# Kernel optimization log

Measured on AMD Instinct MI355X. Metric: run time of the kernel, lower is better.

The kernel has to match this reference:

```python
import jax, jax.numpy as jnp
import numpy as np

# -------- problem dimensions (match init_kwargs / input_specs) --------
B, N, D = 4, 16384, 64          # batch, nodes (=128*128 pixels), feature dim
Q = 128                         # plateau/propagation state width (hardcoded in forward)
W = H = 128                     # grid (hardcoded in forward)
E = 131072                      # edges per batch element
M = 4                           # num_masks = k_nodes - 1
NUM_ITERS = 25                  # GraphPropagator(num_iters=25)
ADJ_THRESH = 0.5                # GraphPropagator(adj_thresh=0.5)


def setup_inputs() -> dict:
    key = jax.random.key(0)
    k1, k2, k3, k4 = jax.random.split(key, 4)
    node_features = jax.random.normal(k1, (B, N, D), dtype=jnp.float32)
    # global node indices in [0, B*N) -- the torch code concatenates per-batch
    # edge lists directly into a (B*N, B*N) SparseTensor
    node_edges = jax.random.randint(k2, (B, 2, E), 0, B * N)
    node_weights = jax.random.uniform(k3, (B, E), dtype=jnp.float32)
    init_state = jax.random.normal(k4, (B, N, Q), dtype=jnp.float32)
    return {"node_features": node_features, "node_edges": node_edges,
            "node_weights": node_weights, "init_state": init_state}


def _propagate(init_state, rows, cols, ws):
    """25-iteration sparse label propagation on the global (B*N,B*N) graph."""
    h = init_state.reshape(B * N, Q)

    def step(h, _):
        msg = ws[:, None] * h[cols]                                  # gather  [B*E, Q]
        agg = jax.ops.segment_sum(msg, rows, num_segments=B * N)    # scatter [B*N, Q]
        hn = agg / (jnp.linalg.norm(agg, axis=-1, keepdims=True) + 1e-8)
        return hn, None

    h, _ = jax.lax.scan(step, h, None, length=NUM_ITERS)
    return h  # [B*N, Q]


def _competition(platmap):
    """Competition(num_masks=M): agents claim pixels by plateau-vector affinity;
    an extra zero-logit background channel yields the unharvested mask."""
    flat = platmap.reshape(B, W * H, Q)
    agent_idx = jnp.linspace(0, W * H - 1, M).astype(jnp.int32)      # deterministic agent pixels
    agents = flat[:, agent_idx, :]                                   # [B, M, Q]
    logits = jnp.einsum('bnq,bmq->bnm', flat, agents) / jnp.sqrt(jnp.float32(Q))
    logits_ext = jnp.concatenate([logits, jnp.zeros((B, W * H, 1), logits.dtype)], axis=-1)
    probs = jax.nn.softmax(logits_ext, axis=-1)                      # [B, WH, M+1]
    masks = probs[..., :M].reshape(B, W, H, M)
    unharv = probs[..., M:].reshape(B, W, H, 1)
    alive = jnp.ones((B, M, 1), dtype=platmap.dtype)
    pheno = agents
    return masks, agents, alive, pheno, unharv


def reference(node_features, node_edges, node_weights, init_state):
    rows = node_edges[:, 0, :].reshape(-1)                           # [B*E] global row idx
    cols = node_edges[:, 1, :].reshape(-1)
    ws = node_weights.reshape(-1)
    ws = jnp.where(ws > ADJ_THRESH, ws, jnp.float32(0.0))            # adjacency threshold

    prop = _propagate(init_state, rows, cols, ws)                    # [B*N, Q]
    platmap = prop.reshape(B, W, H, Q)

    masks, agents, alive, pheno, unharv = _competition(platmap)
    masks_ext = jnp.concatenate([masks, unharv], axis=-1)            # [B, W, H, M+1]
    masks_ext = jnp.transpose(masks_ext, (0, 3, 1, 2))               # [B, M+1, W, H]

    nf = jnp.einsum('bnd,bmn->bmd', node_features,
                    masks_ext.reshape(B, M + 1, W * H))              # [B, M+1, D]
    # F.normalize(p=2, dim=1, eps=1e-12)
    nf = nf / jnp.clip(jnp.linalg.norm(nf, axis=1, keepdims=True), 1e-12)
    node_scores = jnp.max(masks_ext, axis=(-1, -2))                  # [B, M+1]
    return nf, masks_ext, node_scores
```

## Files before the change

### kernel.cpp

```cpp
#include <hip/hip_runtime.h>

#define B_    4
#define N_    16384
#define D_    64
#define Q_    128
#define E_    131072
#define M_    4
#define BN    65536
#define TOTE  524288
#define ITERS 25
#define PAD_CAP (TOTE + 3 * BN + 64)

#define OFF_MASKS 1280
#define OFF_SCORES 328960

__constant__ int c_agidx[4] = {0, 5461, 10922, 16383};

__device__ __forceinline__ unsigned pack_bf16x2(float x, float y) {
    unsigned ux = __float_as_uint(x);
    unsigned uy = __float_as_uint(y);
    ux = (ux + 0x7fffu + ((ux >> 16) & 1u)) >> 16;
    uy = (uy + 0x7fffu + ((uy >> 16) & 1u)) & 0xffff0000u;
    return ux | uy;
}

__global__ void k_count(const int* __restrict__ edges, const float* __restrict__ wts,
                        int* __restrict__ deg) {
    int idx = blockIdx.x * blockDim.x + threadIdx.x;
    if (idx >= TOTE) return;
    int b = idx >> 17;
    int e = idx & (E_ - 1);
    float w = wts[idx];
    if (w > 0.5f) {
        int row = edges[(b * 2) * E_ + e];
        atomicAdd(&deg[row], 1);
    }
}

__global__ __launch_bounds__(256) void k_scan1(const int* __restrict__ deg,
                                               int* __restrict__ blockSums) {
    int i = blockIdx.x * 256 + threadIdx.x;
    int v = (deg[i] + 3) & ~3;
    #pragma unroll
    for (int off = 1; off < 64; off <<= 1) v += __shfl_xor(v, off, 64);
    __shared__ int ws[4];
    int lane = threadIdx.x & 63, w = threadIdx.x >> 6;
    if (lane == 0) ws[w] = v;
    __syncthreads();
    if (threadIdx.x == 0)
        blockSums[blockIdx.x] = ws[0] + ws[1] + ws[2] + ws[3];
}

__global__ __launch_bounds__(256) void k_scan3(const int* __restrict__ deg,
                                               const int* __restrict__ blockSums,
                                               int* __restrict__ row_start,
                                               int* __restrict__ cursor) {
    int t = threadIdx.x;
    int lane = t & 63, w = t >> 6;
    __shared__ int offs[256];
    __shared__ int wtotA[4];
    __shared__ int wtotB[4];

    int bs = blockSums[t];
    int binc = bs;
    #pragma unroll
    for (int off = 1; off < 64; off <<= 1) {
        int u = __shfl_up(binc, off, 64);
        if (lane >= off) binc += u;
    }
    if (lane == 63) wtotA[w] = binc;
    __syncthreads();
    int badd = 0;
    for (int j = 0; j < w; ++j) badd += wtotA[j];
    offs[t] = binc + badd - bs;
    if (blockIdx.x == 0 && t == 255) row_start[BN] = binc + badd;
    __syncthreads();
    int blockOff = offs[blockIdx.x];

    int i = blockIdx.x * 256 + t;
    int v = (deg[i] + 3) & ~3;
    int incl = v;
    #pragma unroll
    for (int off = 1; off < 64; off <<= 1) {
        int u = __shfl_up(incl, off, 64);
        if (lane >= off) incl += u;
    }
    if (lane == 63) wtotB[w] = incl;
    __syncthreads();
    int wadd = 0;
    for (int j = 0; j < w; ++j) wadd += wtotB[j];
    int rs = blockOff + wadd + incl - v;
    row_start[i] = rs;
    cursor[i] = rs;
}

__global__ void k_scatter(const int* __restrict__ edges, const float* __restrict__ wts,
                          int* __restrict__ cursor, int2* __restrict__ cw) {
    int idx = blockIdx.x * blockDim.x + threadIdx.x;
    if (idx >= TOTE) return;
    int b = idx >> 17;
    int e = idx & (E_ - 1);
    float w = wts[idx];
    if (w > 0.5f) {
        int row = edges[(b * 2) * E_ + e];
        int col = edges[(b * 2) * E_ + E_ + e];
        int pos = atomicAdd(&cursor[row], 1);
        cw[pos] = make_int2(col, __float_as_int(w));
    }
}

__global__ void k_sort(const int* __restrict__ row_start, const int* __restrict__ deg,
                       int2* __restrict__ cw) {
    int n = blockIdx.x * blockDim.x + threadIdx.x;
    if (n >= BN) return;
    int s = row_start[n], epos = s + deg[n], pend = row_start[n + 1];
    for (int i = s + 1; i < epos; ++i) {
        int2 v = cw[i];
        unsigned long long key =
            ((unsigned long long)(unsigned)v.x << 32) | (unsigned)v.y;
        int j = i - 1;
        while (j >= s) {
            int2 u = cw[j];
            unsigned long long kj =
                ((unsigned long long)(unsigned)u.x << 32) | (unsigned)u.y;
            if (kj <= key) break;
            cw[j + 1] = u;
            --j;
        }
        cw[j + 1] = v;
    }
    for (int i = epos; i < pend; ++i) cw[i] = make_int2(0, 0);
}

__global__ __launch_bounds__(256) void k_hist(const int* __restrict__ deg,
                                              int* __restrict__ hist) {
    __shared__ int lh[256];
    int t = threadIdx.x;
    lh[t] = 0;
    __syncthreads();
    int n = blockIdx.x * 256 + t;
    int c = (deg[n] + 3) >> 2;
    if (c > 255) c = 255;
    atomicAdd(&lh[c], 1);
    __syncthreads();
    int cnt = lh[t];
    if (cnt) atomicAdd(&hist[t], cnt);
}

__global__ __launch_bounds__(256) void k_bucketscan(const int* __restrict__ hist,
                                                    int* __restrict__ bucketCur) {
    int t = threadIdx.x;
    int lane = t & 63, w = t >> 6;
    int v = hist[t];
    int incl = v;
    #pragma unroll
    for (int off = 1; off < 64; off <<= 1) {
        int u = __shfl_up(incl, off, 64);
        if (lane >= off) incl += u;
    }
    __shared__ int wtot[4];
    if (lane == 63) wtot[w] = incl;
    __syncthreads();
    int wadd = 0;
    for (int j = 0; j < w; ++j) wadd += wtot[j];
    bucketCur[t] = incl + wadd - v;
}

__global__ __launch_bounds__(256) void k_permscatter(const int* __restrict__ deg,
                                                     int* __restrict__ bucketCur,
                                                     int* __restrict__ perm) {
    __shared__ int lh[256];
    __shared__ int lbase[256];
    int t = threadIdx.x;
    lh[t] = 0;
    __syncthreads();
    int n = blockIdx.x * 256 + t;
    int c = (deg[n] + 3) >> 2;
    if (c > 255) c = 255;
    int lpos = atomicAdd(&lh[c], 1);
    __syncthreads();
    int cnt = lh[t];
    lbase[t] = cnt ? atomicAdd(&bucketCur[t], cnt) : 0;
    __syncthreads();
    perm[lbase[c] + lpos] = n;
}

__global__ __launch_bounds__(256) void k_pscan1(const int* __restrict__ deg,
                                                const int* __restrict__ perm,
                                                int* __restrict__ blockSums2) {
    int i = blockIdx.x * 256 + threadIdx.x;
    int v = (deg[perm[i]] + 3) & ~3;
    #pragma unroll
    for (int off = 1; off < 64; off <<= 1) v += __shfl_xor(v, off, 64);
    __shared__ int ws[4];
    int lane = threadIdx.x & 63, w = threadIdx.x >> 6;
    if (lane == 0) ws[w] = v;
    __syncthreads();
    if (threadIdx.x == 0)
        blockSums2[blockIdx.x] = ws[0] + ws[1] + ws[2] + ws[3];
}

__global__ __launch_bounds__(256) void k_pscan3(const int* __restrict__ deg,
                                                const int* __restrict__ perm,
                                                const int* __restrict__ blockSums2,
                                                int* __restrict__ prow) {
    int t = threadIdx.x;
    int lane = t & 63, w = t >> 6;
    __shared__ int offs[256];
    __shared__ int wtotA[4];
    __shared__ int wtotB[4];

    int bs = blockSums2[t];
    int binc = bs;
    #pragma unroll
    for (int off = 1; off < 64; off <<= 1) {
        int u = __shfl_up(binc, off, 64);
        if (lane >= off) binc += u;
    }
    if (lane == 63) wtotA[w] = binc;
    __syncthreads();
    int badd = 0;
    for (int j = 0; j < w; ++j) badd += wtotA[j];
    offs[t] = binc + badd - bs;
    if (blockIdx.x == 0 && t == 255) prow[BN] = binc + badd;
    __syncthreads();
    int blockOff = offs[blockIdx.x];

    int i = blockIdx.x * 256 + t;
    int v = (deg[perm[i]] + 3) & ~3;
    int incl = v;
    #pragma unroll
    for (int off = 1; off < 64; off <<= 1) {
        int u = __shfl_up(incl, off, 64);
        if (lane >= off) incl += u;
    }
    if (lane == 63) wtotB[w] = incl;
    __syncthreads();
    int wadd = 0;
    for (int j = 0; j < w; ++j) wadd += wtotB[j];
    prow[i] = blockOff + wadd + incl - v;
}

__global__ __launch_bounds__(256) void k_copy(const int* __restrict__ row_start,
                                              const int* __restrict__ prow,
                                              const int* __restrict__ perm,
                                              const int* __restrict__ deg,
                                              const int2* __restrict__ cw,
                                              int2* __restrict__ cw2) {
    int i = blockIdx.x * 256 + threadIdx.x;
    int n = perm[i];
    int src = row_start[n];
    int dst = prow[i];
    int nq = (deg[n] + 3) >> 2;
    for (int j = 0; j < nq; ++j) {
        const int4* s = (const int4*)(cw + src + (j << 2));
        int4* d = (int4*)(cw2 + dst + (j << 2));
        int4 x0 = s[0], x1 = s[1];
        d[0] = x0; d[1] = x1;
    }
}

template <bool F32IN>
__global__ __launch_bounds__(256) void k_prop(const void* __restrict__ hin,
                                              unsigned* __restrict__ hout,
                                              const int* __restrict__ prow,
                                              const int2* __restrict__ cw,
                                              const int* __restrict__ perm) {
    int lane = threadIdx.x & 63;
    int gid = (blockIdx.x << 2) + (threadIdx.x >> 6);
    int base = __builtin_amdgcn_readfirstlane(gid << 2);
    const int4 p4 = *(const int4*)(perm + base);
    int u0 = __builtin_amdgcn_readfirstlane(p4.x);
    int u1 = __builtin_amdgcn_readfirstlane(p4.y);
    int u2 = __builtin_amdgcn_readfirstlane(p4.z);
    int u3 = __builtin_amdgcn_readfirstlane(p4.w);
    int s0 = prow[base], s1 = prow[base + 1], s2 = prow[base + 2],
        s3 = prow[base + 3], e3 = prow[base + 4];
    int c0 = (s1 - s0) >> 2, c1 = (s2 - s1) >> 2;
    int c2 = (s3 - s2) >> 2, c3 = (e3 - s3) >> 2;
    int m01 = c0 > c1 ? c0 : c1, m23 = c2 > c3 ? c2 : c3;
    int nmax = m01 > m23 ? m01 : m23;
    int b0 = c0 ? s0 : 0, b1 = c1 ? s1 : 0, b2 = c2 ? s2 : 0, b3 = c3 ? s3 : 0;
    int l0 = (c0 ? c0 : 1) - 1, l1 = (c1 ? c1 : 1) - 1;
    int l2 = (c2 ? c2 : 1) - 1, l3 = (c3 ? c3 : 1) - 1;

    auto gather = [&](int col) -> float2 {
        if constexpr (F32IN) {
            return ((const float2*)hin)[((size_t)col << 6) + lane];
        } else {
            unsigned p = ((const unsigned*)hin)[((size_t)col << 6) + lane];
            float2 r;
            r.x = __uint_as_float(p << 16);
            r.y = __uint_as_float(p & 0xffff0000u);
            return r;
        }
    };

    float ax0 = 0.f, ay0 = 0.f, ax1 = 0.f, ay1 = 0.f;
    float ax2 = 0.f, ay2 = 0.f, ax3 = 0.f, ay3 = 0.f;
    for (int j = 0; j < nmax; ++j) {
        int j0 = j < l0 ? j : l0, j1 = j < l1 ? j : l1;
        int j2 = j < l2 ? j : l2, j3 = j < l3 ? j : l3;
        const int4* q0 = (const int4*)(cw + b0 + (j0 << 2));
        const int4* q1 = (const int4*)(cw + b1 + (j1 << 2));
        const int4* q2 = (const int4*)(cw + b2 + (j2 << 2));
        const int4* q3 = (const int4*)(cw + b3 + (j3 << 2));
        int4 a0 = q0[0], a1 = q0[1];
        int4 a2 = q1[0], a3 = q1[1];
        int4 a4 = q2[0], a5 = q2[1];
        int4 a6 = q3[0], a7 = q3[1];
        float2 v00 = gather(a0.x), v01 = gather(a0.z);
        float2 v02 = gather(a1.x), v03 = gather(a1.z);
        float2 v10 = gather(a2.x), v11 = gather(a2.z);
        float2 v12 = gather(a3.x), v13 = gather(a3.z);
        float2 v20 = gather(a4.x), v21 = gather(a4.z);
        float2 v22 = gather(a5.x), v23 = gather(a5.z);
        float2 v30 = gather(a6.x), v31 = gather(a6.z);
        float2 v32 = gather(a7.x), v33 = gather(a7.z);
        bool k0 = j < c0, k1 = j < c1, k2 = j < c2, k3 = j < c3;
        float w00 = k0 ? __int_as_float(a0.y) : 0.f;
        float w01 = k0 ? __int_as_float(a0.w) : 0.f;
        float w02 = k0 ? __int_as_float(a1.y) : 0.f;
        float w03 = k0 ? __int_as_float(a1.w) : 0.f;
        float w10 = k1 ? __int_as_float(a2.y) : 0.f;
        float w11 = k1 ? __int_as_float(a2.w) : 0.f;
        float w12 = k1 ? __int_as_float(a3.y) : 0.f;
        float w13 = k1 ? __int_as_float(a3.w) : 0.f;
        float w20 = k2 ? __int_as_float(a4.y) : 0.f;
        float w21 = k2 ? __int_as_float(a4.w) : 0.f;
        float w22 = k2 ? __int_as_float(a5.y) : 0.f;
        float w23 = k2 ? __int_as_float(a5.w) : 0.f;
        float w30 = k3 ? __int_as_float(a6.y) : 0.f;
        float w31 = k3 ? __int_as_float(a6.w) : 0.f;
        float w32 = k3 ? __int_as_float(a7.y) : 0.f;
        float w33 = k3 ? __int_as_float(a7.w) : 0.f;
        ax0 = fmaf(w00, v00.x, ax0); ay0 = fmaf(w00, v00.y, ay0);
        ax0 = fmaf(w01, v01.x, ax0); ay0 = fmaf(w01, v01.y, ay0);
        ax0 = fmaf(w02, v02.x, ax0); ay0 = fmaf(w02, v02.y, ay0);
        ax0 = fmaf(w03, v03.x, ax0); ay0 = fmaf(w03, v03.y, ay0);
        ax1 = fmaf(w10, v10.x, ax1); ay1 = fmaf(w10, v10.y, ay1);
        ax1 = fmaf(w11, v11.x, ax1); ay1 = fmaf(w11, v11.y, ay1);
        ax1 = fmaf(w12, v12.x, ax1); ay1 = fmaf(w12, v12.y, ay1);
        ax1 = fmaf(w13, v13.x, ax1); ay1 = fmaf(w13, v13.y, ay1);
        ax2 = fmaf(w20, v20.x, ax2); ay2 = fmaf(w20, v20.y, ay2);
        ax2 = fmaf(w21, v21.x, ax2); ay2 = fmaf(w21, v21.y, ay2);
        ax2 = fmaf(w22, v22.x, ax2); ay2 = fmaf(w22, v22.y, ay2);
        ax2 = fmaf(w23, v23.x, ax2); ay2 = fmaf(w23, v23.y, ay2);
        ax3 = fmaf(w30, v30.x, ax3); ay3 = fmaf(w30, v30.y, ay3);
        ax3 = fmaf(w31, v31.x, ax3); ay3 = fmaf(w31, v31.y, ay3);
        ax3 = fmaf(w32, v32.x, ax3); ay3 = fmaf(w32, v32.y, ay3);
        ax3 = fmaf(w33, v33.x, ax3); ay3 = fmaf(w33, v33.y, ay3);
    }
    float ss0 = ax0 * ax0 + ay0 * ay0;
    float ss1 = ax1 * ax1 + ay1 * ay1;
    float ss2 = ax2 * ax2 + ay2 * ay2;
    float ss3 = ax3 * ax3 + ay3 * ay3;
    #pragma unroll
    for (int off = 32; off; off >>= 1) {
        ss0 += __shfl_xor(ss0, off, 64);
        ss1 += __shfl_xor(ss1, off, 64);
        ss2 += __shfl_xor(ss2, off, 64);
        ss3 += __shfl_xor(ss3, off, 64);
    }
    float i0 = 1.0f / (sqrtf(ss0) + 1e-8f);
    float i1 = 1.0f / (sqrtf(ss1) + 1e-8f);
    float i2 = 1.0f / (sqrtf(ss2) + 1e-8f);
    float i3 = 1.0f / (sqrtf(ss3) + 1e-8f);
    hout[((size_t)u0 << 6) + lane] = pack_bf16x2(ax0 * i0, ay0 * i0);
    hout[((size_t)u1 << 6) + lane] = pack_bf16x2(ax1 * i1, ay1 * i1);
    hout[((size_t)u2 << 6) + lane] = pack_bf16x2(ax2 * i2, ay2 * i2);
    hout[((size_t)u3 << 6) + lane] = pack_bf16x2(ax3 * i3, ay3 * i3);
}

__global__ __launch_bounds__(256) void k_masks(const unsigned* __restrict__ h,
                                               float* __restrict__ masks) {
    int wave = threadIdx.x >> 6;
    int lane = threadIdx.x & 63;
    int n = blockIdx.x * 4 + wave;
    int b = n >> 14;
    int nl = n & (N_ - 1);
    unsigned vp = h[((size_t)n << 6) + lane];
    float vx = __uint_as_float(vp << 16);
    float vy = __uint_as_float(vp & 0xffff0000u);
    float dot[4];
    #pragma unroll
    for (int m = 0; m < 4; ++m) {
        int an = b * N_ + c_agidx[m];
        unsigned ap = h[((size_t)an << 6) + lane];
        float axx = __uint_as_float(ap << 16);
        float ayy = __uint_as_float(ap & 0xffff0000u);
        float d = vx * axx + vy * ayy;
        #pragma unroll
        for (int off = 32; off; off >>= 1) d += __shfl_xor(d, off, 64);
        dot[m] = d;
    }
    const float scl = 0.0883883476483184405501055452631f;
    float l0 = dot[0] * scl, l1 = dot[1] * scl, l2 = dot[2] * scl, l3 = dot[3] * scl;
    float mx = fmaxf(fmaxf(fmaxf(l0, l1), fmaxf(l2, l3)), 0.f);
    float e0 = expf(l0 - mx), e1 = expf(l1 - mx), e2 = expf(l2 - mx),
          e3 = expf(l3 - mx), e4 = expf(0.f - mx);
    float den = e0 + e1 + e2 + e3 + e4;
    if (lane < 5) {
        float p = (lane == 0) ? e0 : (lane == 1) ? e1 : (lane == 2) ? e2
                  : (lane == 3) ? e3 : e4;
        masks[((size_t)b * 5 + lane) * N_ + nl] = p / den;
    }
}

__global__ __launch_bounds__(256) void k_nfpart(const float* __restrict__ feat,
                                                const float* __restrict__ masks,
                                                float* __restrict__ part,
                                                float* __restrict__ maxpart) {
    int b = blockIdx.x >> 6;
    int chunk = blockIdx.x & 63;
    int d = threadIdx.x & 63;
    int g = threadIdx.x >> 6;
    int n0 = chunk * 256 + g * 64;
    const float* fb = feat + (size_t)b * N_ * D_;
    float acc[5] = {0.f, 0.f, 0.f, 0.f, 0.f};
    float mxv[5] = {-1e30f, -1e30f, -1e30f, -1e30f, -1e30f};
    for (int i = 0; i < 64; ++i) {
        int n = n0 + i;
        float fv = fb[(size_t)n * D_ + d];
        #pragma unroll
        for (int m = 0; m < 5; ++m) {
            float mv = masks[((size_t)b * 5 + m) * N_ + n];
            acc[m] = fmaf(fv, mv, acc[m]);
            mxv[m] = fmaxf(mxv[m], mv);
        }
    }
    __shared__ float lds[4][5][64];
    __shared__ float lmx[4][5];
    #pragma unroll
    for (int m = 0; m < 5; ++m) lds[g][m][d] = acc[m];
    if (d == 0) {
        #pragma unroll
        for (int m = 0; m < 5; ++m) lmx[g][m] = mxv[m];
    }
    __syncthreads();
    if (g == 0) {
        #pragma unroll
        for (int m = 0; m < 5; ++m) {
            float s = lds[0][m][d] + lds[1][m][d] + lds[2][m][d] + lds[3][m][d];
            part[(((size_t)b * 64 + chunk) * 5 + m) * 64 + d] = s;
            if (d == 0)
                maxpart[((size_t)b * 64 + chunk) * 5 + m] =
                    fmaxf(fmaxf(lmx[0][m], lmx[1][m]), fmaxf(lmx[2][m], lmx[3][m]));
        }
    }
}

__global__ void k_nffinal(const float* __restrict__ part, const float* __restrict__ maxpart,
                          float* __restrict__ out) {
    int b = blockIdx.x;
    int d = threadIdx.x;
    float v[5];
    float ss = 0.f;
    for (int m = 0; m < 5; ++m) {
        float s = 0.f;
        for (int c = 0; c < 64; ++c)
            s += part[(((size_t)b * 64 + c) * 5 + m) * 64 + d];
        v[m] = s;
        ss += s * s;
    }
    float nrm = fmaxf(sqrtf(ss), 1e-12f);
    for (int m = 0; m < 5; ++m) out[((size_t)b * 5 + m) * 64 + d] = v[m] / nrm;
    if (d < 5) {
        float mx = -1e30f;
        for (int c = 0; c < 64; ++c)
            mx = fmaxf(mx, maxpart[((size_t)b * 64 + c) * 5 + d]);
        out[OFF_SCORES + b * 5 + d] = mx;
    }
}

extern "C" void kernel_launch(void* const* d_in, const int* in_sizes, int n_in,
                              void* d_out, int out_size, void* d_ws, size_t ws_size,
                              hipStream_t stream) {
    const float* feat  = (const float*)d_in[0];
    const int*   edges = (const int*)d_in[1];
    const float* wts   = (const float*)d_in[2];
    const float* init  = (const float*)d_in[3];
    float* out = (float*)d_out;

    unsigned* hA = (unsigned*)d_ws;
    unsigned* hB = hA + (size_t)BN * 64;
    int* row_start  = (int*)(hB + (size_t)BN * 64);
    int* cursor     = row_start + 65544;
    int* deg        = cursor + BN;
    int* hist       = deg + BN;
    int* blockSums  = hist + 256;
    int* blockSums2 = blockSums + 256;
    int* bucketCur  = blockSums2 + 256;
    int* perm       = bucketCur + 256;
    int* prow       = perm + BN;
    int2* cw        = (int2*)(prow + 65544);
    int2* cw2       = cw + PAD_CAP;
    float* part     = (float*)(cw2 + PAD_CAP);
    float* maxpart  = part + 81920;

    hipMemsetAsync(deg, 0, (BN + 256) * sizeof(int), stream);
    k_count<<<TOTE / 256, 256, 0, stream>>>(edges, wts, deg);
    k_scan1<<<256, 256, 0, stream>>>(deg, blockSums);
    k_scan3<<<256, 256, 0, stream>>>(deg, blockSums, row_start, cursor);
    k_scatter<<<TOTE / 256, 256, 0, stream>>>(edges, wts, cursor, cw);
    k_sort<<<BN / 256, 256, 0, stream>>>(row_start, deg, cw);
    k_hist<<<BN / 256, 256, 0, stream>>>(deg, hist);
    k_bucketscan<<<1, 256, 0, stream>>>(hist, bucketCur);
    k_permscatter<<<BN / 256, 256, 0, stream>>>(deg, bucketCur, perm);
    k_pscan1<<<256, 256, 0, stream>>>(deg, perm, blockSums2);
    k_pscan3<<<256, 256, 0, stream>>>(deg, perm, blockSums2, prow);
    k_copy<<<BN / 256, 256, 0, stream>>>(row_start, prow, perm, deg, cw, cw2);

    k_prop<true><<<BN / 16, 256, 0, stream>>>(init, hA, prow, cw2, perm);
    const unsigned* src = hA;
    for (int it = 1; it < ITERS; ++it) {
        unsigned* dst = (it & 1) ? hB : hA;
        k_prop<false><<<BN / 16, 256, 0, stream>>>(src, dst, prow, cw2, perm);
        src = dst;
    }

    k_masks<<<BN / 4, 256, 0, stream>>>(src, out + OFF_MASKS);
    k_nfpart<<<4 * 64, 256, 0, stream>>>(feat, out + OFF_MASKS, part, maxpart);
    k_nffinal<<<4, 64, 0, stream>>>(part, maxpart, out);
}
```

Baseline: 558.2 us.

## Store propagation state in degree-sorted order and process two rows per wave

Builds an inverse permutation and rewrites the edge column indices into permuted node space. The hidden state is then stored in sorted order, so each wave writes contiguous rows and no per-row perm lookup is needed; the first iteration uses the original indices because it reads the unpermuted init state. Each wave now handles 2 rows instead of 4, which doubles the grid and halves register pressure but gives fewer independent gathers in flight per wave. The mask kernel maps node ids through inv. The cost is an extra edge copy plus inverse-index gathers during setup.

```diff
diff --git a/kernel.cpp b/kernel.cpp
--- a/kernel.cpp
+++ b/kernel.cpp
@@ -185,6 +185,11 @@
     perm[lbase[c] + lpos] = n;
 }
 
+__global__ void k_inv(const int* __restrict__ perm, int* __restrict__ inv) {
+    int i = blockIdx.x * 256 + threadIdx.x;
+    inv[perm[i]] = i;
+}
+
 __global__ __launch_bounds__(256) void k_pscan1(const int* __restrict__ deg,
                                                 const int* __restrict__ perm,
                                                 int* __restrict__ blockSums2) {
@@ -245,8 +250,10 @@
                                               const int* __restrict__ prow,
                                               const int* __restrict__ perm,
                                               const int* __restrict__ deg,
+                                              const int* __restrict__ inv,
                                               const int2* __restrict__ cw,
-                                              int2* __restrict__ cw2) {
+                                              int2* __restrict__ cw2,
+                                              int2* __restrict__ cw2o) {
     int i = blockIdx.x * 256 + threadIdx.x;
     int n = perm[i];
     int src = row_start[n];
@@ -254,9 +261,14 @@
     int nq = (deg[n] + 3) >> 2;
     for (int j = 0; j < nq; ++j) {
         const int4* s = (const int4*)(cw + src + (j << 2));
-        int4* d = (int4*)(cw2 + dst + (j << 2));
         int4 x0 = s[0], x1 = s[1];
-        d[0] = x0; d[1] = x1;
+        int4 r0 = x0, r1 = x1;
+        r0.x = inv[x0.x]; r0.z = inv[x0.z];
+        r1.x = inv[x1.x]; r1.z = inv[x1.z];
+        ((int4*)(cw2 + dst + (j << 2)))[0] = r0;
+        ((int4*)(cw2 + dst + (j << 2)))[1] = r1;
+        ((int4*)(cw2o + dst + (j << 2)))[0] = x0;
+        ((int4*)(cw2o + dst + (j << 2)))[1] = x1;
     }
 }
 
@@ -264,25 +276,17 @@
 __global__ __launch_bounds__(256) void k_prop(const void* __restrict__ hin,
                                               unsigned* __restrict__ hout,
                                               const int* __restrict__ prow,
-                                              const int2* __restrict__ cw,
-                                              const int* __restrict__ perm) {
+                                              const int2* __restrict__ cwp) {
     int lane = threadIdx.x & 63;
-    int gid = (blockIdx.x << 2) + (threadIdx.x >> 6);
-    int base = __builtin_amdgcn_readfirstlane(gid << 2);
-    const int4 p4 = *(const int4*)(perm + base);
-    int u0 = __builtin_amdgcn_readfirstlane(p4.x);
-    int u1 = __builtin_amdgcn_readfirstlane(p4.y);
-    int u2 = __builtin_amdgcn_readfirstlane(p4.z);
-    int u3 = __builtin_amdgcn_readfirstlane(p4.w);
-    int s0 = prow[base], s1 = prow[base + 1], s2 = prow[base + 2],
-        s3 = prow[base + 3], e3 = prow[base + 4];
-    int c0 = (s1 - s0) >> 2, c1 = (s2 - s1) >> 2;
-    int c2 = (s3 - s2) >> 2, c3 = (e3 - s3) >> 2;
-    int m01 = c0 > c1 ? c0 : c1, m23 = c2 > c3 ? c2 : c3;
-    int nmax = m01 > m23 ? m01 : m23;
-    int b0 = c0 ? s0 : 0, b1 = c1 ? s1 : 0, b2 = c2 ? s2 : 0, b3 = c3 ? s3 : 0;
-    int l0 = (c0 ? c0 : 1) - 1, l1 = (c1 ? c1 : 1) - 1;
-    int l2 = (c2 ? c2 : 1) - 1, l3 = (c3 ? c3 : 1) - 1;
+    int w = (blockIdx.x << 2) + (threadIdx.x >> 6);
+    int base = __builtin_amdgcn_readfirstlane(w << 1);
+    int sA = prow[base], sB = prow[base + 1], eB = prow[base + 2];
+    int cA = (sB - sA) >> 2, cB = (eB - sB) >> 2;
+    int nmax = cA > cB ? cA : cB;
+    int baseA = cA ? sA : sB;
+    int baseB = cB ? sB : sA;
+    int lastA = (cA ? cA : 1) - 1;
+    int lastB = (cB ? cB : 1) - 1;
 
     auto gather = [&](int col) -> float2 {
         if constexpr (F32IN) {
@@ -296,96 +300,70 @@
         }
     };
 
-    float ax0 = 0.f, ay0 = 0.f, ax1 = 0.f, ay1 = 0.f;
-    float ax2 = 0.f, ay2 = 0.f, ax3 = 0.f, ay3 = 0.f;
+    float axA = 0.f, ayA = 0.f, axB = 0.f, ayB = 0.f;
     for (int j = 0; j < nmax; ++j) {
-        int j0 = j < l0 ? j : l0, j1 = j < l1 ? j : l1;
-        int j2 = j < l2 ? j : l2, j3 = j < l3 ? j : l3;
-        const int4* q0 = (const int4*)(cw + b0 + (j0 << 2));
-        const int4* q1 = (const int4*)(cw + b1 + (j1 << 2));
-        const int4* q2 = (const int4*)(cw + b2 + (j2 << 2));
-        const int4* q3 = (const int4*)(cw + b3 + (j3 << 2));
-        int4 a0 = q0[0], a1 = q0[1];
-        int4 a2 = q1[0], a3 = q1[1];
-        int4 a4 = q2[0], a5 = q2[1];
-        int4 a6 = q3[0], a7 = q3[1];
-        float2 v00 = gather(a0.x), v01 = gather(a0.z);
-        float2 v02 = gather(a1.x), v03 = gather(a1.z);
-        float2 v10 = gather(a2.x), v11 = gather(a2.z);
-        float2 v12 = gather(a3.x), v13 = gather(a3.z);
-        float2 v20 = gather(a4.x), v21 = gather(a4.z);
-        float2 v22 = gather(a5.x), v23 = gather(a5.z);
-        float2 v30 = gather(a6.x), v31 = gather(a6.z);
-        float2 v32 = gather(a7.x), v33 = gather(a7.z);
-        bool k0 = j < c0, k1 = j < c1, k2 = j < c2, k3 = j < c3;
-        float w00 = k0 ? __int_as_float(a0.y) : 0.f;
-        float w01 = k0 ? __int_as_float(a0.w) : 0.f;
-        float w02 = k0 ? __int_as_float(a1.y) : 0.f;
-        float w03 = k0 ? __int_as_float(a1.w) : 0.f;
-        float w10 = k1 ? __int_as_float(a2.y) : 0.f;
-        float w11 = k1 ? __int_as_float(a2.w) : 0.f;
-        float w12 = k1 ? __int_as_float(a3.y) : 0.f;
-        float w13 = k1 ? __int_as_float(a3.w) : 0.f;
-        float w20 = k2 ? __int_as_float(a4.y) : 0.f;
-        float w21 = k2 ? __int_as_float(a4.w) : 0.f;
-        float w22 = k2 ? __int_as_float(a5.y) : 0.f;
-        float w23 = k2 ? __int_as_float(a5.w) : 0.f;
-        float w30 = k3 ? __int_as_float(a6.y) : 0.f;
-        float w31 = k3 ? __int_as_float(a6.w) : 0.f;
-        float w32 = k3 ? __int_as_float(a7.y) : 0.f;
-        float w33 = k3 ? __int_as_float(a7.w) : 0.f;
-        ax0 = fmaf(w00, v00.x, ax0); ay0 = fmaf(w00, v00.y, ay0);
-        ax0 = fmaf(w01, v01.x, ax0); ay0 = fmaf(w01, v01.y, ay0);
-        ax0 = fmaf(w02, v02.x, ax0); ay0 = fmaf(w02, v02.y, ay0);
-        ax0 = fmaf(w03, v03.x, ax0); ay0 = fmaf(w03, v03.y, ay0);
-        ax1 = fmaf(w10, v10.x, ax1); ay1 = fmaf(w10, v10.y, ay1);
-        ax1 = fmaf(w11, v11.x, ax1); ay1 = fmaf(w11, v11.y, ay1);
-        ax1 = fmaf(w12, v12.x, ax1); ay1 = fmaf(w12, v12.y, ay1);
-        ax1 = fmaf(w13, v13.x, ax1); ay1 = fmaf(w13, v13.y, ay1);
-        ax2 = fmaf(w20, v20.x, ax2); ay2 = fmaf(w20, v20.y, ay2);
-        ax2 = fmaf(w21, v21.x, ax2); ay2 = fmaf(w21, v21.y, ay2);
-        ax2 = fmaf(w22, v22.x, ax2); ay2 = fmaf(w22, v22.y, ay2);
-        ax2 = fmaf(w23, v23.x, ax2); ay2 = fmaf(w23, v23.y, ay2);
-        ax3 = fmaf(w30, v30.x, ax3); ay3 = fmaf(w30, v30.y, ay3);
-        ax3 = fmaf(w31, v31.x, ax3); ay3 = fmaf(w31, v31.y, ay3);
-        ax3 = fmaf(w32, v32.x, ax3); ay3 = fmaf(w32, v32.y, ay3);
-        ax3 = fmaf(w33, v33.x, ax3); ay3 = fmaf(w33, v33.y, ay3);
-    }
-    float ss0 = ax0 * ax0 + ay0 * ay0;
-    float ss1 = ax1 * ax1 + ay1 * ay1;
-    float ss2 = ax2 * ax2 + ay2 * ay2;
-    float ss3 = ax3 * ax3 + ay3 * ay3;
+        int jA = j < lastA ? j : lastA;
+        int jB = j < lastB ? j : lastB;
+        const int4* qA = (const int4*)(cwp + baseA + (jA << 2));
+        const int4* qB = (const int4*)(cwp + baseB + (jB << 2));
+        int4 a0 = qA[0], a1 = qA[1];
+        int4 b0 = qB[0], b1 = qB[1];
+        float2 vA0 = gather(a0.x);
+        float2 vA1 = gather(a0.z);
+        float2 vA2 = gather(a1.x);
+        float2 vA3 = gather(a1.z);
+        float2 vB0 = gather(b0.x);
+        float2 vB1 = gather(b0.z);
+        float2 vB2 = gather(b1.x);
+        float2 vB3 = gather(b1.z);
+        bool okA = j < cA, okB = j < cB;
+        float wA0 = okA ? __int_as_float(a0.y) : 0.f;
+        float wA1 = okA ? __int_as_float(a0.w) : 0.f;
+        float wA2 = okA ? __int_as_float(a1.y) : 0.f;
+        float wA3 = okA ? __int_as_float(a1.w) : 0.f;
+        float wB0 = okB ? __int_as_float(b0.y) : 0.f;
+        float wB1 = okB ? __int_as_float(b0.w) : 0.f;
+        float wB2 = okB ? __int_as_float(b1.y) : 0.f;
+        float wB3 = okB ? __int_as_float(b1.w) : 0.f;
+        axA = fmaf(wA0, vA0.x, axA); ayA = fmaf(wA0, vA0.y, ayA);
+        axA = fmaf(wA1, vA1.x, axA); ayA = fmaf(wA1, vA1.y, ayA);
+        axA = fmaf(wA2, vA2.x, axA); ayA = fmaf(wA2, vA2.y, ayA);
+        axA = fmaf(wA3, vA3.x, axA); ayA = fmaf(wA3, vA3.y, ayA);
+        axB = fmaf(wB0, vB0.x, axB); ayB = fmaf(wB0, vB0.y, ayB);
+        axB = fmaf(wB1, vB1.x, axB); ayB = fmaf(wB1, vB1.y, ayB);
+        axB = fmaf(wB2, vB2.x, axB); ayB = fmaf(wB2, vB2.y, ayB);
+        axB = fmaf(wB3, vB3.x, axB); ayB = fmaf(wB3, vB3.y, ayB);
+    }
+    float ssA = axA * axA + ayA * ayA;
+    float ssB = axB * axB + ayB * ayB;
     #pragma unroll
     for (int off = 32; off; off >>= 1) {
-        ss0 += __shfl_xor(ss0, off, 64);
-        ss1 += __shfl_xor(ss1, off, 64);
-        ss2 += __shfl_xor(ss2, off, 64);
-        ss3 += __shfl_xor(ss3, off, 64);
-    }
-    float i0 = 1.0f / (sqrtf(ss0) + 1e-8f);
-    float i1 = 1.0f / (sqrtf(ss1) + 1e-8f);
-    float i2 = 1.0f / (sqrtf(ss2) + 1e-8f);
-    float i3 = 1.0f / (sqrtf(ss3) + 1e-8f);
-    hout[((size_t)u0 << 6) + lane] = pack_bf16x2(ax0 * i0, ay0 * i0);
-    hout[((size_t)u1 << 6) + lane] = pack_bf16x2(ax1 * i1, ay1 * i1);
-    hout[((size_t)u2 << 6) + lane] = pack_bf16x2(ax2 * i2, ay2 * i2);
-    hout[((size_t)u3 << 6) + lane] = pack_bf16x2(ax3 * i3, ay3 * i3);
+        ssA += __shfl_xor(ssA, off, 64);
+        ssB += __shfl_xor(ssB, off, 64);
+    }
+    float invA = 1.0f / (sqrtf(ssA) + 1e-8f);
+    float invB = 1.0f / (sqrtf(ssB) + 1e-8f);
+    hout[((size_t)base << 6) + lane] = pack_bf16x2(axA * invA, ayA * invA);
+    hout[((size_t)(base + 1) << 6) + lane] = pack_bf16x2(axB * invB, ayB * invB);
 }
 
 __global__ __launch_bounds__(256) void k_masks(const unsigned* __restrict__ h,
+                                               const int* __restrict__ inv,
                                                float* __restrict__ masks) {
     int wave = threadIdx.x >> 6;
     int lane = threadIdx.x & 63;
     int n = blockIdx.x * 4 + wave;
-    int b = n >> 14;
-    int nl = n & (N_ - 1);
-    unsigned vp = h[((size_t)n << 6) + lane];
+    int un = __builtin_amdgcn_readfirstlane(n);
+    int b = un >> 14;
+    int nl = un & (N_ - 1);
+    int rn = inv[un];
+    unsigned vp = h[((size_t)rn << 6) + lane];
     float vx = __uint_as_float(vp << 16);
     float vy = __uint_as_float(vp & 0xffff0000u);
     float dot[4];
     #pragma unroll
     for (int m = 0; m < 4; ++m) {
-        int an = b * N_ + c_agidx[m];
+        int an = inv[b * N_ + c_agidx[m]];
         unsigned ap = h[((size_t)an << 6) + lane];
         float axx = __uint_as_float(ap << 16);
         float ayy = __uint_as_float(ap & 0xffff0000u);
@@ -492,10 +470,12 @@
     int* blockSums2 = blockSums + 256;
     int* bucketCur  = blockSums2 + 256;
     int* perm       = bucketCur + 256;
-    int* prow       = perm + BN;
+    int* inv        = perm + BN;
+    int* prow       = inv + BN;
     int2* cw        = (int2*)(prow + 65544);
     int2* cw2       = cw + PAD_CAP;
-    float* part     = (float*)(cw2 + PAD_CAP);
+    int2* cw2o      = cw2 + PAD_CAP;
+    float* part     = (float*)(cw2o + PAD_CAP);
     float* maxpart  = part + 81920;
 
     hipMemsetAsync(deg, 0, (BN + 256) * sizeof(int), stream);
@@ -507,19 +487,20 @@
     k_hist<<<BN / 256, 256, 0, stream>>>(deg, hist);
     k_bucketscan<<<1, 256, 0, stream>>>(hist, bucketCur);
     k_permscatter<<<BN / 256, 256, 0, stream>>>(deg, bucketCur, perm);
+    k_inv<<<BN / 256, 256, 0, stream>>>(perm, inv);
     k_pscan1<<<256, 256, 0, stream>>>(deg, perm, blockSums2);
     k_pscan3<<<256, 256, 0, stream>>>(deg, perm, blockSums2, prow);
-    k_copy<<<BN / 256, 256, 0, stream>>>(row_start, prow, perm, deg, cw, cw2);
-
-    k_prop<true><<<BN / 16, 256, 0, stream>>>(init, hA, prow, cw2, perm);
+    k_copy<<<BN / 256, 256, 0, stream>>>(row_start, prow, perm, deg, inv, cw, cw2, cw2o);
+
+    k_prop<true><<<BN / 8, 256, 0, stream>>>(init, hA, prow, cw2o);
     const unsigned* src = hA;
     for (int it = 1; it < ITERS; ++it) {
         unsigned* dst = (it & 1) ? hB : hA;
-        k_prop<false><<<BN / 16, 256, 0, stream>>>(src, dst, prow, cw2, perm);
+        k_prop<false><<<BN / 8, 256, 0, stream>>>(src, dst, prow, cw2);
         src = dst;
     }
 
-    k_masks<<<BN / 4, 256, 0, stream>>>(src, out + OFF_MASKS);
+    k_masks<<<BN / 4, 256, 0, stream>>>(src, inv, out + OFF_MASKS);
     k_nfpart<<<4 * 64, 256, 0, stream>>>(feat, out + OFF_MASKS, part, maxpart);
     k_nffinal<<<4, 64, 0, stream>>>(part, maxpart, out);
 }
```

Result: faster. 535.7 us (-4.0%).
